# Optimization experiments

Hardware: AMD Instinct MI355X
Metric: run time of the kernel (lower is better)

Reference implementation:

```python
import jax, jax.numpy as jnp
import numpy as np

H_OUT = 512
W_OUT = 512


def _leaky(x):
    return jnp.where(x >= 0, x, 0.2 * x)


def _spline(cp, out_size):
    # cp: [B, R, N] control points -> [B, R, out_size] cubic Hermite interp
    N = cp.shape[-1]
    nseg = N - 1
    eps = 1e-3
    t = jnp.linspace(eps, 1.0 - eps, out_size)
    ts = t * nseg
    seg = jnp.clip(jnp.floor(ts).astype(jnp.int32), 0, nseg - 1)
    tau = jnp.clip(ts - seg.astype(ts.dtype), 0.0, 0.9999)
    t2 = tau * tau
    t3 = t2 * tau
    h00 = 2 * t3 - 3 * t2 + 1
    h10 = t3 - 2 * t2 + tau
    h01 = -2 * t3 + 3 * t2
    h11 = t3 - t2
    # central-difference tangents, scaled by 1/num_segments
    m = jnp.concatenate([
        (cp[..., 1:2] - cp[..., 0:1]) * 0.5,
        (cp[..., 2:] - cp[..., :-2]) * 0.5,
        (cp[..., -1:] - cp[..., -2:-1]) * 0.5,
    ], axis=-1) / nseg
    seg1 = jnp.clip(seg + 1, 0, N - 1)
    pk = cp[..., seg]
    pk1 = cp[..., seg1]
    mk = m[..., seg]
    mk1 = m[..., seg1]
    return h00 * pk + h10 * mk + h01 * pk1 + h11 * mk1


def _gen(feats, w1, b1, w2, b2):
    # batched per-rank 2-layer MLP: feats [B,R,D], w1 [R,D,Hd], w2 [R,Hd,C]
    hdn = _leaky(jnp.einsum('brd,rdh->brh', feats, w1) + b1[None])
    return jnp.einsum('brh,rhc->brc', hdn, w2) + b2[None]


def setup_inputs() -> dict:
    key = jax.random.key(0)
    ks = iter(jax.random.split(key, 40))
    def rn(shape, s=0.05):
        return jax.random.normal(next(ks), shape, jnp.float32) * s
    B, D, Hd = 64, 768, 256
    Rm, Ra, CX, CY = 16, 8, 24, 24
    Rt = Rm + Ra
    inp = {
        'h': jax.random.normal(next(ks), (B, D), jnp.float32),
        'rank_emb': rn((Rt, Hd), 0.1),
        'st_w1': rn((D, 2 * Hd)), 'st_b1': jnp.zeros((2 * Hd,), jnp.float32),
        'st_w2': rn((2 * Hd, Hd)), 'st_b2': jnp.zeros((Hd,), jnp.float32),
        'rm_w1': rn((Rt, 2 * Hd, Hd)), 'rm_b1': jnp.zeros((Rt, Hd), jnp.float32),
        'rm_w2': rn((Rt, Hd, Hd)), 'rm_b2': jnp.zeros((Rt, Hd), jnp.float32),
        'mx_w1': rn((Rm, Hd, Hd)), 'mx_b1': jnp.zeros((Rm, Hd), jnp.float32),
        'mx_w2': rn((Rm, Hd, CX)), 'mx_b2': jnp.zeros((Rm, CX), jnp.float32),
        'my_w1': rn((Rm, Hd, Hd)), 'my_b1': jnp.zeros((Rm, Hd), jnp.float32),
        'my_w2': rn((Rm, Hd, CY)), 'my_b2': jnp.zeros((Rm, CY), jnp.float32),
        'ax_w1': rn((Ra, Hd, Hd)), 'ax_b1': jnp.zeros((Ra, Hd), jnp.float32),
        'ax_w2': rn((Ra, Hd, CX)), 'ax_b2': jnp.zeros((Ra, CX), jnp.float32),
        'ay_w1': rn((Ra, Hd, Hd)), 'ay_b1': jnp.zeros((Ra, Hd), jnp.float32),
        'ay_w2': rn((Ra, Hd, CY)), 'ay_b2': jnp.zeros((Ra, CY), jnp.float32),
        'mult_w': jnp.ones((Rm,), jnp.float32) / Rm,
        'addx_w': jnp.ones((Ra,), jnp.float32) / Ra * 0.5,
        'addy_w': jnp.ones((Ra,), jnp.float32) / Ra * 0.5,
        'gbias': jnp.asarray(0.5, jnp.float32),
    }
    return inp


def reference(h, rank_emb, st_w1, st_b1, st_w2, st_b2,
              rm_w1, rm_b1, rm_w2, rm_b2,
              mx_w1, mx_b1, mx_w2, mx_b2,
              my_w1, my_b1, my_w2, my_b2,
              ax_w1, ax_b1, ax_w2, ax_b2,
              ay_w1, ay_b1, ay_w2, ay_b2,
              mult_w, addx_w, addy_w, gbias):
    B = h.shape[0]
    Rt = rank_emb.shape[0]
    Rm = mx_w1.shape[0]
    # shared conditioning
    shared = _leaky(h @ st_w1 + st_b1) @ st_w2 + st_b2  # [B, Hd]
    comb = jnp.concatenate([
        jnp.broadcast_to(shared[:, None, :], (B, Rt, shared.shape[-1])),
        jnp.broadcast_to(rank_emb[None], (B, Rt, rank_emb.shape[-1])),
    ], axis=-1)  # [B, Rt, 2*Hd]
    rf = _gen(comb, rm_w1, rm_b1, rm_w2, rm_b2)  # [B, Rt, Hd]
    fm, fa = rf[:, :Rm], rf[:, Rm:]
    Px_m = _gen(fm, mx_w1, mx_b1, mx_w2, mx_b2)  # [B, Rm, CX]
    Py_m = _gen(fm, my_w1, my_b1, my_w2, my_b2)
    Px_a = _gen(fa, ax_w1, ax_b1, ax_w2, ax_b2)
    Py_a = _gen(fa, ay_w1, ay_b1, ay_w2, ay_b2)
    u = _spline(Px_m, W_OUT)   # [B, Rm, W]
    v = _spline(Py_m, H_OUT)   # [B, Rm, H]
    a_x = _spline(Px_a, W_OUT)
    b_y = _spline(Py_a, H_OUT)
    depth_mult = jnp.einsum('brw,brh,r->bhw', u, v, jax.nn.softmax(mult_w))
    dx = jnp.einsum('brw,r->bw', a_x, jax.nn.softmax(addx_w))
    dy = jnp.einsum('brh,r->bh', b_y, jax.nn.softmax(addy_w))
    depth = depth_mult + dx[:, None, :] + dy[:, :, None] + gbias
    return depth[:, None]  # [B, 1, H, W]
```

## Files before the change

kernel.cpp:

```cpp
#include <hip/hip_runtime.h>


__device__ __forceinline__ float leaky(float v) { return v >= 0.f ? v : 0.2f * v; }

__global__ __launch_bounds__(256, 2) void l1_kernel(
    const float* __restrict__ h, const float* __restrict__ W,
    const float* __restrict__ bias, float* __restrict__ outp)
{
    __shared__ __align__(16) float a_lds[128][34];
    __shared__ __align__(16) float w_lds[128][34];
    const int tid = threadIdx.x;
    const int x = blockIdx.x, z = blockIdx.z;
    const int b0 = (x & 1) * 32, n0 = (x >> 1) * 32;
    const int nq = tid & 15, bq = tid >> 4;
    const int k0 = z * 128;
    float a00, a01, a10, a11;
    if (z == 0) {
        float bv0 = bias[n0 + nq * 2], bv1 = bias[n0 + nq * 2 + 1];
        a00 = bv0; a01 = bv1; a10 = bv0; a11 = bv1;
    } else { a00 = a01 = a10 = a11 = 0.f; }
    #pragma unroll
    for (int j = 0; j < 16; ++j) {
        int idx = tid + j * 256;
        int k = idx & 127, c = idx >> 7;
        a_lds[k][c] = h[(size_t)(b0 + c) * 768 + k0 + k];
        int n = idx & 31, kk = idx >> 5;
        w_lds[kk][n] = W[(size_t)(k0 + kk) * 512 + n0 + n];
    }
    __syncthreads();
    #pragma unroll 32
    for (int kk = 0; kk < 128; ++kk) {
        float2 a = *(const float2*)&a_lds[kk][bq * 2];
        float2 w = *(const float2*)&w_lds[kk][nq * 2];
        a00 += a.x * w.x; a01 += a.x * w.y;
        a10 += a.y * w.x; a11 += a.y * w.y;
    }
    float* ob = outp + (size_t)z * 32768;
    ob[(size_t)(b0 + bq * 2) * 512 + n0 + nq * 2]         = a00;
    ob[(size_t)(b0 + bq * 2) * 512 + n0 + nq * 2 + 1]     = a01;
    ob[(size_t)(b0 + bq * 2 + 1) * 512 + n0 + nq * 2]     = a10;
    ob[(size_t)(b0 + bq * 2 + 1) * 512 + n0 + nq * 2 + 1] = a11;
}

__global__ __launch_bounds__(512, 1) void mega_kernel(
    const float* __restrict__ hid1p,
    const float* __restrict__ st_w2, const float* __restrict__ st_b2,
    const float* __restrict__ rank_emb,
    const float* __restrict__ rm_w1, const float* __restrict__ rm_b1,
    const float* __restrict__ rm_w2, const float* __restrict__ rm_b2,
    const float* __restrict__ mx_w1, const float* __restrict__ mx_b1,
    const float* __restrict__ mx_w2, const float* __restrict__ mx_b2,
    const float* __restrict__ my_w1, const float* __restrict__ my_b1,
    const float* __restrict__ my_w2, const float* __restrict__ my_b2,
    const float* __restrict__ ax_w1, const float* __restrict__ ax_b1,
    const float* __restrict__ ax_w2, const float* __restrict__ ax_b2,
    const float* __restrict__ ay_w1, const float* __restrict__ ay_b1,
    const float* __restrict__ ay_w2, const float* __restrict__ ay_b2,
    float* __restrict__ Pcat)
{
    __shared__ __align__(16) float hid_s[8][512];
    __shared__ __align__(16) float sh_s[8][256];
    __shared__ __align__(16) float hdn_s[8][256];
    __shared__ __align__(16) float rf_s[8][256];
    __shared__ __align__(16) float hc_s[2][8][256];
    __shared__ float re_s[256];
    __shared__ float remb_s[256];
    const int tid = threadIdx.x;
    const int blk = blockIdx.x;
    const int r = blk % 24;
    const int bt = blk / 24;
    const int b0 = bt * 8;
    const int col = tid & 255, rh = tid >> 8;
    const int r0 = rh * 4;

    {
        const float4* hp = (const float4*)hid1p;
        #pragma unroll
        for (int i = 0; i < 2; ++i) {
            int idx = tid + i * 512;
            int row = idx >> 7, j4 = idx & 127;
            size_t off = (size_t)(b0 + row) * 128 + j4;
            float4 v0 = hp[off],            v1 = hp[8192 + off],  v2 = hp[16384 + off];
            float4 v3 = hp[24576 + off],    v4 = hp[32768 + off], v5 = hp[40960 + off];
            float4 s;
            s.x = leaky(v0.x + v1.x + v2.x + v3.x + v4.x + v5.x);
            s.y = leaky(v0.y + v1.y + v2.y + v3.y + v4.y + v5.y);
            s.z = leaky(v0.z + v1.z + v2.z + v3.z + v4.z + v5.z);
            s.w = leaky(v0.w + v1.w + v2.w + v3.w + v4.w + v5.w);
            ((float4*)&hid_s[row][0])[j4] = s;
        }
    }
    if (tid < 256) remb_s[tid] = rank_emb[r * 256 + tid];
    __syncthreads();

    {
        float bv = st_b2[col];
        float a0 = bv, a1 = bv, a2 = bv, a3 = bv;
        const float* wp = st_w2 + col;
        #pragma unroll 4
        for (int d = 0; d < 512; d += 4) {
            float w0 = wp[(size_t)(d + 0) * 256], w1 = wp[(size_t)(d + 1) * 256];
            float w2 = wp[(size_t)(d + 2) * 256], w3 = wp[(size_t)(d + 3) * 256];
            float4 s0 = *(const float4*)&hid_s[r0 + 0][d];
            float4 s1 = *(const float4*)&hid_s[r0 + 1][d];
            float4 s2 = *(const float4*)&hid_s[r0 + 2][d];
            float4 s3 = *(const float4*)&hid_s[r0 + 3][d];
            a0 += s0.x * w0 + s0.y * w1 + s0.z * w2 + s0.w * w3;
            a1 += s1.x * w0 + s1.y * w1 + s1.z * w2 + s1.w * w3;
            a2 += s2.x * w0 + s2.y * w1 + s2.z * w2 + s2.w * w3;
            a3 += s3.x * w0 + s3.y * w1 + s3.z * w2 + s3.w * w3;
        }
        sh_s[r0 + 0][col] = a0; sh_s[r0 + 1][col] = a1;
        sh_s[r0 + 2][col] = a2; sh_s[r0 + 3][col] = a3;
    }
    __syncthreads();

    if (tid < 256) {
        float rb = rm_b1[r * 256 + col];
        const float* wb = rm_w1 + ((size_t)r * 512 + 256) * 256 + col;
        #pragma unroll 4
        for (int d = 0; d < 256; d += 4) {
            float w0 = wb[(size_t)(d + 0) * 256], w1 = wb[(size_t)(d + 1) * 256];
            float w2 = wb[(size_t)(d + 2) * 256], w3 = wb[(size_t)(d + 3) * 256];
            float4 e = *(const float4*)&remb_s[d];
            rb += e.x * w0 + e.y * w1 + e.z * w2 + e.w * w3;
        }
        re_s[col] = rb;
    }
    __syncthreads();

    {
        float bv = re_s[col];
        float a0 = bv, a1 = bv, a2 = bv, a3 = bv;
        const float* wp = rm_w1 + (size_t)r * 512 * 256 + col;
        #pragma unroll 4
        for (int d = 0; d < 256; d += 4) {
            float w0 = wp[(size_t)(d + 0) * 256], w1 = wp[(size_t)(d + 1) * 256];
            float w2 = wp[(size_t)(d + 2) * 256], w3 = wp[(size_t)(d + 3) * 256];
            float4 s0 = *(const float4*)&sh_s[r0 + 0][d];
            float4 s1 = *(const float4*)&sh_s[r0 + 1][d];
            float4 s2 = *(const float4*)&sh_s[r0 + 2][d];
            float4 s3 = *(const float4*)&sh_s[r0 + 3][d];
            a0 += s0.x * w0 + s0.y * w1 + s0.z * w2 + s0.w * w3;
            a1 += s1.x * w0 + s1.y * w1 + s1.z * w2 + s1.w * w3;
            a2 += s2.x * w0 + s2.y * w1 + s2.z * w2 + s2.w * w3;
            a3 += s3.x * w0 + s3.y * w1 + s3.z * w2 + s3.w * w3;
        }
        hdn_s[r0 + 0][col] = leaky(a0); hdn_s[r0 + 1][col] = leaky(a1);
        hdn_s[r0 + 2][col] = leaky(a2); hdn_s[r0 + 3][col] = leaky(a3);
    }
    __syncthreads();

    {
        float bv = rm_b2[r * 256 + col];
        float a0 = bv, a1 = bv, a2 = bv, a3 = bv;
        const float* wp = rm_w2 + (size_t)r * 65536 + col;
        #pragma unroll 4
        for (int d = 0; d < 256; d += 4) {
            float w0 = wp[(size_t)(d + 0) * 256], w1 = wp[(size_t)(d + 1) * 256];
            float w2 = wp[(size_t)(d + 2) * 256], w3 = wp[(size_t)(d + 3) * 256];
            float4 s0 = *(const float4*)&hdn_s[r0 + 0][d];
            float4 s1 = *(const float4*)&hdn_s[r0 + 1][d];
            float4 s2 = *(const float4*)&hdn_s[r0 + 2][d];
            float4 s3 = *(const float4*)&hdn_s[r0 + 3][d];
            a0 += s0.x * w0 + s0.y * w1 + s0.z * w2 + s0.w * w3;
            a1 += s1.x * w0 + s1.y * w1 + s1.z * w2 + s1.w * w3;
            a2 += s2.x * w0 + s2.y * w1 + s2.z * w2 + s2.w * w3;
            a3 += s3.x * w0 + s3.y * w1 + s3.z * w2 + s3.w * w3;
        }
        rf_s[r0 + 0][col] = a0; rf_s[r0 + 1][col] = a1;
        rf_s[r0 + 2][col] = a2; rf_s[r0 + 3][col] = a3;
    }
    __syncthreads();

    const float *W1, *B1, *W2, *B2; int y;
    if (r < 16) {
        if (rh == 0) { y = r;      W1 = mx_w1 + (size_t)r * 65536;  B1 = mx_b1 + r * 256;  W2 = mx_w2 + (size_t)r * 6144;  B2 = mx_b2 + r * 24; }
        else         { y = 16 + r; W1 = my_w1 + (size_t)r * 65536;  B1 = my_b1 + r * 256;  W2 = my_w2 + (size_t)r * 6144;  B2 = my_b2 + r * 24; }
    } else {
        int rw = r - 16;
        if (rh == 0) { y = 32 + rw; W1 = ax_w1 + (size_t)rw * 65536; B1 = ax_b1 + rw * 256; W2 = ax_w2 + (size_t)rw * 6144; B2 = ax_b2 + rw * 24; }
        else         { y = 40 + rw; W1 = ay_w1 + (size_t)rw * 65536; B1 = ay_b1 + rw * 256; W2 = ay_w2 + (size_t)rw * 6144; B2 = ay_b2 + rw * 24; }
    }

    {
        float bv = B1[col];
        float acc[8];
        #pragma unroll
        for (int i = 0; i < 8; ++i) acc[i] = bv;
        const float* wp = W1 + col;
        #pragma unroll 2
        for (int d = 0; d < 256; d += 4) {
            float w0 = wp[(size_t)(d + 0) * 256], w1 = wp[(size_t)(d + 1) * 256];
            float w2 = wp[(size_t)(d + 2) * 256], w3 = wp[(size_t)(d + 3) * 256];
            #pragma unroll
            for (int i = 0; i < 8; ++i) {
                float4 s = *(const float4*)&rf_s[i][d];
                acc[i] += s.x * w0 + s.y * w1 + s.z * w2 + s.w * w3;
            }
        }
        #pragma unroll
        for (int i = 0; i < 8; ++i) hc_s[rh][i][col] = leaky(acc[i]);
    }
    __syncthreads();

    if (col < 192) {
        int row = col / 24, cj = col - row * 24;
        float acc = B2[cj];
        const float* wp = W2 + cj;
        #pragma unroll 4
        for (int d = 0; d < 256; d += 4) {
            float w0 = wp[(size_t)(d + 0) * 24], w1 = wp[(size_t)(d + 1) * 24];
            float w2 = wp[(size_t)(d + 2) * 24], w3 = wp[(size_t)(d + 3) * 24];
            float4 s = *(const float4*)&hc_s[rh][row][d];
            acc += s.x * w0 + s.y * w1 + s.z * w2 + s.w * w3;
        }
        Pcat[(size_t)(b0 + row) * 1152 + y * 24 + cj] = acc;
    }
}

__global__ __launch_bounds__(256, 2) void depth_fused_kernel(
    const float* __restrict__ Pcat,
    const float* __restrict__ mult_w, const float* __restrict__ addx_w,
    const float* __restrict__ addy_w, const float* __restrict__ gbias,
    float* __restrict__ out)
{
    __shared__ float cp[48][25];
    __shared__ float sw[33];
    __shared__ __align__(16) float u_s[16][132];
    __shared__ __align__(16) float v_s[16][132];
    __shared__ float dx_s[128], dy_s[128];
    const int tid = threadIdx.x;
    const int b = blockIdx.z, h0 = blockIdx.y * 128, w0 = blockIdx.x * 128;
    for (int idx = tid; idx < 1152; idx += 256)
        cp[idx / 24][idx % 24] = Pcat[(size_t)b * 1152 + idx];
    if (tid == 0) {
        float e[16], m, s;
        m = -1e30f; for (int i = 0; i < 16; ++i) m = fmaxf(m, mult_w[i]);
        s = 0.f;    for (int i = 0; i < 16; ++i) { e[i] = __expf(mult_w[i] - m); s += e[i]; }
        for (int i = 0; i < 16; ++i) sw[i] = e[i] / s;
        m = -1e30f; for (int i = 0; i < 8; ++i) m = fmaxf(m, addx_w[i]);
        s = 0.f;    for (int i = 0; i < 8; ++i) { e[i] = __expf(addx_w[i] - m); s += e[i]; }
        for (int i = 0; i < 8; ++i) sw[16 + i] = e[i] / s;
        m = -1e30f; for (int i = 0; i < 8; ++i) m = fmaxf(m, addy_w[i]);
        s = 0.f;    for (int i = 0; i < 8; ++i) { e[i] = __expf(addy_w[i] - m); s += e[i]; }
        for (int i = 0; i < 8; ++i) sw[24 + i] = e[i] / s;
        sw[32] = gbias[0];
    }
    __syncthreads();
    {
        const int local = tid & 127;
        const int gpos = (tid < 128 ? w0 : h0) + local;
        const float eps = 0.001f;
        float t = eps + (float)gpos * ((1.f - 2.f * eps) / 511.f);
        float ts = t * 23.f;
        int seg = (int)ts; if (seg > 22) seg = 22;
        float tau = ts - (float)seg;
        tau = fminf(fmaxf(tau, 0.f), 0.9999f);
        float t2 = tau * tau, t3 = t2 * tau;
        float h00 = 2.f * t3 - 3.f * t2 + 1.f;
        float h10 = t3 - 2.f * t2 + tau;
        float h01 = -2.f * t3 + 3.f * t2;
        float h11 = t3 - t2;
        int sm1 = seg > 0 ? seg - 1 : 0;
        int s1 = seg + 1;
        int sp2 = s1 < 23 ? s1 + 1 : 23;
        const float msc = 0.5f / 23.f;
        auto spl = [&](int row) -> float {
            float pk = cp[row][seg], pk1 = cp[row][s1];
            float mk  = msc * (pk1 - cp[row][sm1]);
            float mk1 = msc * (cp[row][sp2] - pk);
            return h00 * pk + h10 * mk + h01 * pk1 + h11 * mk1;
        };
        if (tid < 128) {
            #pragma unroll
            for (int r = 0; r < 16; ++r) u_s[r][local] = sw[r] * spl(r);
            float dx = sw[32];
            #pragma unroll
            for (int r = 0; r < 8; ++r) dx += sw[16 + r] * spl(32 + r);
            dx_s[local] = dx;
        } else {
            #pragma unroll
            for (int r = 0; r < 16; ++r) v_s[r][local] = spl(16 + r);
            float dy = 0.f;
            #pragma unroll
            for (int r = 0; r < 8; ++r) dy += sw[24 + r] * spl(40 + r);
            dy_s[local] = dy;
        }
    }
    __syncthreads();
    const int tw = tid & 15, th = tid >> 4;
    float acc[8][8];
    #pragma unroll
    for (int i = 0; i < 8; ++i)
        #pragma unroll
        for (int j = 0; j < 8; ++j) acc[i][j] = 0.f;
    #pragma unroll
    for (int r = 0; r < 16; ++r) {
        float4 va0 = *(const float4*)&v_s[r][th * 8];
        float4 va1 = *(const float4*)&v_s[r][th * 8 + 4];
        float4 ub0 = *(const float4*)&u_s[r][tw * 8];
        float4 ub1 = *(const float4*)&u_s[r][tw * 8 + 4];
        float va[8] = {va0.x, va0.y, va0.z, va0.w, va1.x, va1.y, va1.z, va1.w};
        float ub[8] = {ub0.x, ub0.y, ub0.z, ub0.w, ub1.x, ub1.y, ub1.z, ub1.w};
        #pragma unroll
        for (int i = 0; i < 8; ++i)
            #pragma unroll
            for (int j = 0; j < 8; ++j)
                acc[i][j] += va[i] * ub[j];
    }
    #pragma unroll
    for (int i = 0; i < 8; ++i) {
        float dyh = dy_s[th * 8 + i];
        float* op = out + (size_t)b * 262144 + (size_t)(h0 + th * 8 + i) * 512 + w0 + tw * 8;
        float4 o0, o1;
        o0.x = acc[i][0] + dx_s[tw * 8 + 0] + dyh;
        o0.y = acc[i][1] + dx_s[tw * 8 + 1] + dyh;
        o0.z = acc[i][2] + dx_s[tw * 8 + 2] + dyh;
        o0.w = acc[i][3] + dx_s[tw * 8 + 3] + dyh;
        o1.x = acc[i][4] + dx_s[tw * 8 + 4] + dyh;
        o1.y = acc[i][5] + dx_s[tw * 8 + 5] + dyh;
        o1.z = acc[i][6] + dx_s[tw * 8 + 6] + dyh;
        o1.w = acc[i][7] + dx_s[tw * 8 + 7] + dyh;
        *(float4*)op = o0;
        *(float4*)(op + 4) = o1;
    }
}

extern "C" void kernel_launch(void* const* d_in, const int* in_sizes, int n_in,
                              void* d_out, int out_size, void* d_ws, size_t ws_size,
                              hipStream_t stream) {
    const float* in_h     = (const float*)d_in[0];
    const float* rank_emb = (const float*)d_in[1];
    const float* st_w1    = (const float*)d_in[2];
    const float* st_b1    = (const float*)d_in[3];
    const float* st_w2    = (const float*)d_in[4];
    const float* st_b2    = (const float*)d_in[5];
    const float* rm_w1    = (const float*)d_in[6];
    const float* rm_b1    = (const float*)d_in[7];
    const float* rm_w2    = (const float*)d_in[8];
    const float* rm_b2    = (const float*)d_in[9];
    const float* mx_w1    = (const float*)d_in[10];
    const float* mx_b1    = (const float*)d_in[11];
    const float* mx_w2    = (const float*)d_in[12];
    const float* mx_b2    = (const float*)d_in[13];
    const float* my_w1    = (const float*)d_in[14];
    const float* my_b1    = (const float*)d_in[15];
    const float* my_w2    = (const float*)d_in[16];
    const float* my_b2    = (const float*)d_in[17];
    const float* ax_w1    = (const float*)d_in[18];
    const float* ax_b1    = (const float*)d_in[19];
    const float* ax_w2    = (const float*)d_in[20];
    const float* ax_b2    = (const float*)d_in[21];
    const float* ay_w1    = (const float*)d_in[22];
    const float* ay_b1    = (const float*)d_in[23];
    const float* ay_w2    = (const float*)d_in[24];
    const float* ay_b2    = (const float*)d_in[25];
    const float* mult_w   = (const float*)d_in[26];
    const float* addx_w   = (const float*)d_in[27];
    const float* addy_w   = (const float*)d_in[28];
    const float* gbias    = (const float*)d_in[29];
    (void)in_sizes; (void)n_in; (void)out_size; (void)ws_size;

    float* ws = (float*)d_ws;
    float* hid1p = ws;
    float* Pcat  = ws + 196608;

    l1_kernel<<<dim3(32, 1, 6), 256, 0, stream>>>(in_h, st_w1, st_b1, hid1p);

    mega_kernel<<<192, 512, 0, stream>>>(
        hid1p, st_w2, st_b2, rank_emb,
        rm_w1, rm_b1, rm_w2, rm_b2,
        mx_w1, mx_b1, mx_w2, mx_b2,
        my_w1, my_b1, my_w2, my_b2,
        ax_w1, ax_b1, ax_w2, ax_b2,
        ay_w1, ay_b1, ay_w2, ay_b2,
        Pcat);

    depth_fused_kernel<<<dim3(4, 4, 64), 256, 0, stream>>>(
        Pcat, mult_w, addx_w, addy_w, gbias, (float*)d_out);
}
```

Measured before the change: 239.9 us.

## Fuse first shared MLP layer into mega kernel, removing l1 launch

Removes the separate split-K l1_kernel and computes h @ st_w1 + bias with leaky activation inside each mega_kernel block for its 8 batch rows. This drops one kernel launch and the round trip of partial sums through the workspace. In exchange, every one of the 192 blocks recomputes the layer for its rows and re-reads the full 768x512 st_w1 matrix, which is 24x redundant work across the rank dimension, and LDS use grows by 24 KB.

```diff
diff --git a/kernel.cpp b/kernel.cpp
--- a/kernel.cpp
+++ b/kernel.cpp
@@ -3,47 +3,9 @@
 
 __device__ __forceinline__ float leaky(float v) { return v >= 0.f ? v : 0.2f * v; }
 
-__global__ __launch_bounds__(256, 2) void l1_kernel(
-    const float* __restrict__ h, const float* __restrict__ W,
-    const float* __restrict__ bias, float* __restrict__ outp)
-{
-    __shared__ __align__(16) float a_lds[128][34];
-    __shared__ __align__(16) float w_lds[128][34];
-    const int tid = threadIdx.x;
-    const int x = blockIdx.x, z = blockIdx.z;
-    const int b0 = (x & 1) * 32, n0 = (x >> 1) * 32;
-    const int nq = tid & 15, bq = tid >> 4;
-    const int k0 = z * 128;
-    float a00, a01, a10, a11;
-    if (z == 0) {
-        float bv0 = bias[n0 + nq * 2], bv1 = bias[n0 + nq * 2 + 1];
-        a00 = bv0; a01 = bv1; a10 = bv0; a11 = bv1;
-    } else { a00 = a01 = a10 = a11 = 0.f; }
-    #pragma unroll
-    for (int j = 0; j < 16; ++j) {
-        int idx = tid + j * 256;
-        int k = idx & 127, c = idx >> 7;
-        a_lds[k][c] = h[(size_t)(b0 + c) * 768 + k0 + k];
-        int n = idx & 31, kk = idx >> 5;
-        w_lds[kk][n] = W[(size_t)(k0 + kk) * 512 + n0 + n];
-    }
-    __syncthreads();
-    #pragma unroll 32
-    for (int kk = 0; kk < 128; ++kk) {
-        float2 a = *(const float2*)&a_lds[kk][bq * 2];
-        float2 w = *(const float2*)&w_lds[kk][nq * 2];
-        a00 += a.x * w.x; a01 += a.x * w.y;
-        a10 += a.y * w.x; a11 += a.y * w.y;
-    }
-    float* ob = outp + (size_t)z * 32768;
-    ob[(size_t)(b0 + bq * 2) * 512 + n0 + nq * 2]         = a00;
-    ob[(size_t)(b0 + bq * 2) * 512 + n0 + nq * 2 + 1]     = a01;
-    ob[(size_t)(b0 + bq * 2 + 1) * 512 + n0 + nq * 2]     = a10;
-    ob[(size_t)(b0 + bq * 2 + 1) * 512 + n0 + nq * 2 + 1] = a11;
-}
-
 __global__ __launch_bounds__(512, 1) void mega_kernel(
-    const float* __restrict__ hid1p,
+    const float* __restrict__ h_in,
+    const float* __restrict__ st_w1, const float* __restrict__ st_b1,
     const float* __restrict__ st_w2, const float* __restrict__ st_b2,
     const float* __restrict__ rank_emb,
     const float* __restrict__ rm_w1, const float* __restrict__ rm_b1,
@@ -58,6 +20,7 @@
     const float* __restrict__ ay_w2, const float* __restrict__ ay_b2,
     float* __restrict__ Pcat)
 {
+    __shared__ __align__(16) float h_s[8][768];
     __shared__ __align__(16) float hid_s[8][512];
     __shared__ __align__(16) float sh_s[8][256];
     __shared__ __align__(16) float hdn_s[8][256];
@@ -74,23 +37,36 @@
     const int r0 = rh * 4;
 
     {
-        const float4* hp = (const float4*)hid1p;
-        #pragma unroll
-        for (int i = 0; i < 2; ++i) {
+        const float4* hp = (const float4*)h_in;
+        #pragma unroll
+        for (int i = 0; i < 3; ++i) {
             int idx = tid + i * 512;
-            int row = idx >> 7, j4 = idx & 127;
-            size_t off = (size_t)(b0 + row) * 128 + j4;
-            float4 v0 = hp[off],            v1 = hp[8192 + off],  v2 = hp[16384 + off];
-            float4 v3 = hp[24576 + off],    v4 = hp[32768 + off], v5 = hp[40960 + off];
-            float4 s;
-            s.x = leaky(v0.x + v1.x + v2.x + v3.x + v4.x + v5.x);
-            s.y = leaky(v0.y + v1.y + v2.y + v3.y + v4.y + v5.y);
-            s.z = leaky(v0.z + v1.z + v2.z + v3.z + v4.z + v5.z);
-            s.w = leaky(v0.w + v1.w + v2.w + v3.w + v4.w + v5.w);
-            ((float4*)&hid_s[row][0])[j4] = s;
+            int row = idx / 192, j4 = idx - row * 192;
+            ((float4*)&h_s[row][0])[j4] = hp[(size_t)(b0 + row) * 192 + j4];
         }
     }
     if (tid < 256) remb_s[tid] = rank_emb[r * 256 + tid];
+    __syncthreads();
+
+    {
+        float acc[8];
+        float bv = st_b1[tid];
+        #pragma unroll
+        for (int i = 0; i < 8; ++i) acc[i] = bv;
+        const float* wp = st_w1 + tid;
+        #pragma unroll 2
+        for (int d = 0; d < 768; d += 4) {
+            float w0 = wp[(size_t)(d + 0) * 512], w1 = wp[(size_t)(d + 1) * 512];
+            float w2 = wp[(size_t)(d + 2) * 512], w3 = wp[(size_t)(d + 3) * 512];
+            #pragma unroll
+            for (int i = 0; i < 8; ++i) {
+                float4 s = *(const float4*)&h_s[i][d];
+                acc[i] += s.x * w0 + s.y * w1 + s.z * w2 + s.w * w3;
+            }
+        }
+        #pragma unroll
+        for (int i = 0; i < 8; ++i) hid_s[i][tid] = leaky(acc[i]);
+    }
     __syncthreads();
 
     {
@@ -362,14 +338,10 @@
     const float* gbias    = (const float*)d_in[29];
     (void)in_sizes; (void)n_in; (void)out_size; (void)ws_size;
 
-    float* ws = (float*)d_ws;
-    float* hid1p = ws;
-    float* Pcat  = ws + 196608;
-
-    l1_kernel<<<dim3(32, 1, 6), 256, 0, stream>>>(in_h, st_w1, st_b1, hid1p);
+    float* Pcat = (float*)d_ws;
 
     mega_kernel<<<192, 512, 0, stream>>>(
-        hid1p, st_w2, st_b2, rank_emb,
+        in_h, st_w1, st_b1, st_w2, st_b2, rank_emb,
         rm_w1, rm_b1, rm_w2, rm_b2,
         mx_w1, mx_b1, mx_w2, mx_b2,
         my_w1, my_b1, my_w2, my_b2,
```

After: 290.6 us. 21.1% more time.
